# Optimization experiments

Measured on AMD Instinct MI355X. Metric: run time of the kernel, lower is better.

## Reference

```python
import jax, jax.numpy as jnp
import numpy as np

NUM_FACES = 400000  # total SMPL face count; faces[] and pix_to_face values lie in [-1, NUM_FACES)


def setup_inputs() -> dict:
    key = jax.random.key(0)
    k0, k1, k2, k3 = jax.random.split(key, 4)
    V, N, C, S = 4, 200000, 64, 512
    verts = jax.random.normal(k0, (N, 3), jnp.float32) * 0.5
    faces = jax.random.randint(k1, (N,), 0, NUM_FACES)
    # identity cameras looking at the point cloud from z=3 so projections land in-frame
    cam_rot = jnp.broadcast_to(jnp.eye(3, dtype=jnp.float32), (V, 3, 3))
    cam_trans = jnp.tile(jnp.array([0.0, 0.0, 3.0], jnp.float32), (V, 1))
    K = jnp.broadcast_to(
        jnp.array([[400.0, 0.0, 255.5], [0.0, 400.0, 255.5], [0.0, 0.0, 1.0]], jnp.float32),
        (V, 3, 3),
    )
    feature = jax.random.normal(k2, (V, C, S, S), jnp.float32)
    pix_to_face = jax.random.randint(k3, (V, S, S), -1, NUM_FACES).astype(jnp.int32)
    return dict(verts=verts, faces=faces, cam_rot=cam_rot, cam_trans=cam_trans, K=K,
                image_size=S, feature=feature, pix_to_face=pix_to_face)


def _project_xy(verts, K, R, t):
    # verts [N,3] -> pixel coords [N,2]
    cam = verts @ R.T + t  # [N,3]
    pix = cam @ K.T        # [N,3]
    return pix[:, :2] / pix[:, 2:]


def _bilinear_sample(feat, x, y, S):
    # feat [C,S,S]; torch grid_sample bilinear, align_corners=True, zero padding.
    # uv = loc/(S-1)*2-1 then grid_sample maps uv back to pixel coords, so the
    # sample location is exactly (x, y) in pixel space.
    x0 = jnp.floor(x); y0 = jnp.floor(y)
    x1 = x0 + 1.0;     y1 = y0 + 1.0
    wx1 = x - x0; wx0 = 1.0 - wx1
    wy1 = y - y0; wy0 = 1.0 - wy1

    def corner(xi, yi, w):
        valid = (xi >= 0) & (xi <= S - 1) & (yi >= 0) & (yi <= S - 1)
        xc = jnp.clip(xi, 0, S - 1).astype(jnp.int32)
        yc = jnp.clip(yi, 0, S - 1).astype(jnp.int32)
        return feat[:, yc, xc] * (w * valid)[None, :]  # [C,N]

    out = (corner(x0, y0, wx0 * wy0) + corner(x1, y0, wx1 * wy0)
           + corner(x0, y1, wx0 * wy1) + corner(x1, y1, wx1 * wy1))
    return out.T  # [N,C]


def _vis_mask(p2f, faces):
    # p2f [S,S] int (>=0 = foreground face id); faces [N] per-vertex face id.
    # Equivalent to torch.isin(faces, p2f[p2f>=0]) via a scatter membership table.
    flat = p2f.reshape(-1)
    idx = jnp.where(flat >= 0, flat, NUM_FACES)  # route background to sentinel slot
    table = jnp.zeros(NUM_FACES + 1, dtype=bool).at[idx].set(True)
    table = table.at[NUM_FACES].set(False)
    return table[faces]  # [N] bool


def reference(verts, faces, cam_rot, cam_trans, K, image_size, feature, pix_to_face):
    S = image_size

    def per_view(featv, Kv, Rv, tv, p2fv):
        xy = _project_xy(verts, Kv, Rv, tv)                    # [N,2]
        samp = _bilinear_sample(featv, xy[:, 0], xy[:, 1], S)  # [N,C]
        mask = _vis_mask(p2fv, faces)                          # [N]
        return samp, mask

    sampled, vmask = jax.vmap(per_view)(feature, K, cam_rot, cam_trans, pix_to_face)
    vm = vmask.astype(feature.dtype)                 # [V,N]
    # vertices invisible in all views: treat as visible everywhere (weight 1)
    vm = jnp.where(vm.sum(axis=0, keepdims=True) == 0, jnp.ones_like(vm), vm)
    out = (sampled * vm[:, :, None]).sum(axis=0) / vm.sum(axis=0)[:, None]  # [N,C]
    return out
```

## Files before the change

kernel.cpp:

```cpp
#include <hip/hip_runtime.h>

#define NUM_FACES 400000
#define NVIEW 4
#define NCHAN 64
#define IMGS 512
#define XT32 (IMGS / 32)
#define VPW 3

typedef float f32x4 __attribute__((ext_vector_type(4)));
typedef float f32x2 __attribute__((ext_vector_type(2)));

__device__ __forceinline__ unsigned short f2bf(float f) {
    unsigned int u = __float_as_uint(f);
    return (unsigned short)((u + 0x7FFFu + ((u >> 16) & 1u)) >> 16);
}

__device__ __forceinline__ void project_view(
    const float* __restrict__ cam_rot, const float* __restrict__ cam_trans,
    const float* __restrict__ Kmat, int v, float px, float py, float pz,
    float& x, float& y)
{
    const float* R  = cam_rot   + v * 9;
    const float* t  = cam_trans + v * 3;
    const float* Km = Kmat      + v * 9;
    float cx = R[0] * px + R[1] * py + R[2] * pz + t[0];
    float cy = R[3] * px + R[4] * py + R[5] * pz + t[1];
    float cz = R[6] * px + R[7] * py + R[8] * pz + t[2];
    float qx = Km[0] * cx + Km[1] * cy + Km[2] * cz;
    float qy = Km[3] * cx + Km[4] * cy + Km[5] * cz;
    float qz = Km[6] * cx + Km[7] * cy + Km[8] * cz;
    x = qx / qz;
    y = qy / qz;
}

__global__ void zero_ws_kernel(uint4* __restrict__ p, int n16) {
    int i = blockIdx.x * blockDim.x + threadIdx.x;
    if (i < n16) p[i] = make_uint4(0u, 0u, 0u, 0u);
}

__global__ void scatter_vis_kernel(const int4* __restrict__ p2f4,
                                   unsigned char* __restrict__ table) {
    const int pix4 = (NVIEW * IMGS * IMGS) / 4;
    int i = blockIdx.x * blockDim.x + threadIdx.x;
    if (i >= pix4) return;
    int4 f4 = p2f4[i];
    int v = i / ((IMGS * IMGS) / 4);
    unsigned char* tv = table + (size_t)v * NUM_FACES;
    if (f4.x >= 0) tv[f4.x] = 1;
    if (f4.y >= 0) tv[f4.y] = 1;
    if (f4.z >= 0) tv[f4.z] = 1;
    if (f4.w >= 0) tv[f4.w] = 1;
}

__global__ void vprep_kernel(const float* __restrict__ verts,
                             const int* __restrict__ faces,
                             const float* __restrict__ cam_rot,
                             const float* __restrict__ cam_trans,
                             const float* __restrict__ Kmat,
                             const unsigned char* __restrict__ table,
                             float* __restrict__ xyv,
                             unsigned char* __restrict__ vmask,
                             unsigned char* __restrict__ flags,
                             int n_verts) {
    int n = blockIdx.x * blockDim.x + threadIdx.x;
    if (n >= n_verts) return;
    float px = verts[n * 3 + 0], py = verts[n * 3 + 1], pz = verts[n * 3 + 2];
    int f = faces[n];
    unsigned int m = 0;
    float xy[8];
#pragma unroll
    for (int v = 0; v < NVIEW; ++v) {
        float x, y;
        project_view(cam_rot, cam_trans, Kmat, v, px, py, pz, x, y);
        xy[v * 2 + 0] = x;
        xy[v * 2 + 1] = y;
        if (f >= 0 && table[(size_t)v * NUM_FACES + f]) m |= (1u << v);
        int ix0 = (int)floorf(x), iy0 = (int)floorf(y);
        int bx  = min(max(ix0, 0), IMGS - 2);
        int ry0 = min(max(iy0, 0), IMGS - 1);
        int ry1 = min(max(iy0 + 1, 0), IMGS - 1);
        int ta = bx >> 5, tb = (bx + 1) >> 5;
        unsigned char* fv = flags + (size_t)v * IMGS * XT32;
        fv[ry0 * XT32 + ta] = 1;
        if (tb != ta) fv[ry0 * XT32 + tb] = 1;
        fv[ry1 * XT32 + ta] = 1;
        if (tb != ta) fv[ry1 * XT32 + tb] = 1;
    }
    if (m == 0) m = 15u;
    vmask[n] = (unsigned char)m;
    f32x4 a, b;
    a.x = xy[0]; a.y = xy[1]; a.z = xy[2]; a.w = xy[3];
    b.x = xy[4]; b.y = xy[5]; b.z = xy[6]; b.w = xy[7];
    f32x4* xp = reinterpret_cast<f32x4*>(xyv + (size_t)n * 8);
    xp[0] = a;
    xp[1] = b;
}

__global__ __launch_bounds__(256) void transpose_feat_kernel(
    const float* __restrict__ feature,
    unsigned short* __restrict__ feat_t,
    const unsigned char* __restrict__ flags)
{
    int b = blockIdx.x;
    int xt = b % XT32;
    int y  = (b / XT32) % IMGS;
    int v  = b / (XT32 * IMGS);
    if (!flags[((size_t)v * IMGS + y) * XT32 + xt]) return;

    __shared__ float tile[64 * 33];
    int x0 = xt * 32;
    const size_t SS = (size_t)IMGS * IMGS;
    int tid = threadIdx.x;

    const float* src = feature + (size_t)v * NCHAN * SS + (size_t)y * IMGS + x0;
#pragma unroll
    for (int i = 0; i < 2; ++i) {
        int lin = i * 256 + tid;
        int c  = lin >> 3;
        int xq = (lin & 7) * 4;
        f32x4 val = __builtin_nontemporal_load(
            reinterpret_cast<const f32x4*>(src + (size_t)c * SS + xq));
        tile[c * 33 + xq + 0] = val.x;
        tile[c * 33 + xq + 1] = val.y;
        tile[c * 33 + xq + 2] = val.z;
        tile[c * 33 + xq + 3] = val.w;
    }
    __syncthreads();

    unsigned short* dst = feat_t + (((size_t)v * IMGS + y) * IMGS + x0) * NCHAN;
#pragma unroll
    for (int i = 0; i < 2; ++i) {
        int lin = i * 256 + tid;
        int x  = lin >> 4;
        int c0 = (lin & 15) * 4;
        ushort4 w;
        w.x = f2bf(tile[(c0 + 0) * 33 + x]);
        w.y = f2bf(tile[(c0 + 1) * 33 + x]);
        w.z = f2bf(tile[(c0 + 2) * 33 + x]);
        w.w = f2bf(tile[(c0 + 3) * 33 + x]);
        *reinterpret_cast<ushort4*>(dst + (size_t)x * NCHAN + c0) = w;
    }
}

__global__ __launch_bounds__(256) void project_sample_bf16_kernel(
    const float* __restrict__ xyv,
    const unsigned char* __restrict__ vmask,
    const unsigned short* __restrict__ feat_t,
    float* __restrict__ out,
    int n_verts)
{
    int n0 = blockIdx.x * (4 * VPW) + (threadIdx.x >> 6) * VPW;
    int lane  = threadIdx.x & 63;
    int lhalf = lane >> 5;
    int cp    = lane & 31;

    unsigned int m[VPW];
    f32x4 xya[VPW], xyb[VPW];
#pragma unroll
    for (int s = 0; s < VPW; ++s) {
        int n = n0 + s;
        if (n < n_verts) {
            m[s] = vmask[n];
            const f32x4* xp = reinterpret_cast<const f32x4*>(xyv + (size_t)n * 8);
            xya[s] = xp[0];
            xyb[s] = xp[1];
        } else {
            m[s] = 0u;
            xya[s] = 0.f;
            xyb[s] = 0.f;
        }
    }

    unsigned int u0[VPW][NVIEW], u1[VPW][NVIEW];
    float w0[VPW][NVIEW], w1[VPW][NVIEW];
#pragma unroll
    for (int s = 0; s < VPW; ++s) {
        float xs[NVIEW] = {xya[s].x, xya[s].z, xyb[s].x, xyb[s].z};
        float ys[NVIEW] = {xya[s].y, xya[s].w, xyb[s].y, xyb[s].w};
#pragma unroll
        for (int v = 0; v < NVIEW; ++v) {
            u0[s][v] = 0u; u1[s][v] = 0u; w0[s][v] = 0.f; w1[s][v] = 0.f;
            if (m[s] & (1u << v)) {
                float x = xs[v], y = ys[v];
                float x0f = floorf(x), y0f = floorf(y);
                float wx1 = x - x0f, wx0 = 1.f - wx1;
                float wy1 = y - y0f, wy0 = 1.f - wy1;
                int ix0 = (int)x0f, iy0 = (int)y0f;
                int ix1 = ix0 + 1, iy1 = iy0 + 1;

                int bx = min(max(ix0, 0), IMGS - 2);
                int k  = bx + lhalf;
                float wxk = (k == ix0 ? wx0 : 0.f) + (k == ix1 ? wx1 : 0.f);

                int ry0 = min(max(iy0, 0), IMGS - 1);
                int ry1 = min(max(iy1, 0), IMGS - 1);
                float wyr0 = (iy0 >= 0 && iy0 <= IMGS - 1) ? wy0 : 0.f;
                float wyr1 = (iy1 >= 0 && iy1 <= IMGS - 1) ? wy1 : 0.f;

                const unsigned int* fv32 = reinterpret_cast<const unsigned int*>(
                    feat_t + (size_t)v * IMGS * IMGS * NCHAN);
                u0[s][v] = fv32[((size_t)ry0 * IMGS + bx) * 32 + lane];
                u1[s][v] = fv32[((size_t)ry1 * IMGS + bx) * 32 + lane];
                w0[s][v] = wxk * wyr0;
                w1[s][v] = wxk * wyr1;
            }
        }
    }

#pragma unroll
    for (int s = 0; s < VPW; ++s) {
        if (m[s] == 0u) continue;
        float accx = 0.f, accy = 0.f;
#pragma unroll
        for (int v = 0; v < NVIEW; ++v) {
            accx += __uint_as_float(u0[s][v] << 16) * w0[s][v]
                  + __uint_as_float(u1[s][v] << 16) * w1[s][v];
            accy += __uint_as_float(u0[s][v] & 0xFFFF0000u) * w0[s][v]
                  + __uint_as_float(u1[s][v] & 0xFFFF0000u) * w1[s][v];
        }
        accx += __shfl_xor(accx, 32, 64);
        accy += __shfl_xor(accy, 32, 64);
        if (lhalf == 0) {
            float r = 1.f / (float)__popc(m[s]);
            f32x2 o; o.x = accx * r; o.y = accy * r;
            __builtin_nontemporal_store(o,
                reinterpret_cast<f32x2*>(out + (size_t)(n0 + s) * NCHAN) + cp);
        }
    }
}

__global__ __launch_bounds__(256) void project_sample_direct_kernel(
    const float* __restrict__ verts,
    const int* __restrict__ faces,
    const float* __restrict__ cam_rot,
    const float* __restrict__ cam_trans,
    const float* __restrict__ Kmat,
    const float* __restrict__ feature,
    const unsigned char* __restrict__ table,
    float* __restrict__ out,
    int n_verts)
{
    int n = blockIdx.x * 4 + (threadIdx.x >> 6);
    int c = threadIdx.x & 63;
    if (n >= n_verts) return;

    float px = verts[n * 3 + 0], py = verts[n * 3 + 1], pz = verts[n * 3 + 2];
    int f = faces[n];
    float xs[NVIEW], ys[NVIEW], mask[NVIEW];
    float vsum = 0.f;
#pragma unroll
    for (int v = 0; v < NVIEW; ++v) {
        project_view(cam_rot, cam_trans, Kmat, v, px, py, pz, xs[v], ys[v]);
        float mm = (f >= 0 && table[(size_t)v * NUM_FACES + f]) ? 1.f : 0.f;
        mask[v] = mm; vsum += mm;
    }
    float wsum = vsum;
    if (vsum == 0.f) {
#pragma unroll
        for (int v = 0; v < NVIEW; ++v) mask[v] = 1.f;
        wsum = (float)NVIEW;
    }
    float acc = 0.f;
#pragma unroll
    for (int v = 0; v < NVIEW; ++v) {
        if (mask[v] == 0.f) continue;
        float x = xs[v], y = ys[v];
        float x0f = floorf(x), y0f = floorf(y);
        float wx1 = x - x0f, wx0 = 1.f - wx1;
        float wy1 = y - y0f, wy0 = 1.f - wy1;
        int x0 = (int)x0f, y0 = (int)y0f;
        int x1 = x0 + 1, y1 = y0 + 1;
        bool vx0 = (x0 >= 0) && (x0 <= IMGS - 1), vx1 = (x1 >= 0) && (x1 <= IMGS - 1);
        bool vy0 = (y0 >= 0) && (y0 <= IMGS - 1), vy1 = (y1 >= 0) && (y1 <= IMGS - 1);
        int cx0 = min(max(x0, 0), IMGS - 1), cx1 = min(max(x1, 0), IMGS - 1);
        int cy0 = min(max(y0, 0), IMGS - 1), cy1 = min(max(y1, 0), IMGS - 1);
        const float* fc = feature + ((size_t)v * NCHAN + c) * (size_t)(IMGS * IMGS);
        acc += fc[cy0 * IMGS + cx0] * (wx0 * wy0 * (float)(vx0 && vy0))
             + fc[cy0 * IMGS + cx1] * (wx1 * wy0 * (float)(vx1 && vy0))
             + fc[cy1 * IMGS + cx0] * (wx0 * wy1 * (float)(vx0 && vy1))
             + fc[cy1 * IMGS + cx1] * (wx1 * wy1 * (float)(vx1 && vy1));
    }
    out[(size_t)n * NCHAN + c] = acc / wsum;
}

extern "C" void kernel_launch(void* const* d_in, const int* in_sizes, int n_in,
                              void* d_out, int out_size, void* d_ws, size_t ws_size,
                              hipStream_t stream) {
    const float* verts     = (const float*)d_in[0];
    const int*   faces     = (const int*)d_in[1];
    const float* cam_rot   = (const float*)d_in[2];
    const float* cam_trans = (const float*)d_in[3];
    const float* Kmat      = (const float*)d_in[4];
    const float* feature   = (const float*)d_in[6];
    const int4*  p2f4      = (const int4*)d_in[7];
    float* out = (float*)d_out;

    int n_verts = in_sizes[1];

    size_t table_sz  = (size_t)NVIEW * NUM_FACES;
    size_t flag_off  = table_sz;
    size_t flag_sz   = (size_t)NVIEW * IMGS * XT32;
    size_t xyv_off   = (flag_off + flag_sz + 255) & ~(size_t)255;
    size_t xyv_sz    = (size_t)n_verts * 8 * sizeof(float);
    size_t vm_off    = xyv_off + xyv_sz;
    size_t vm_sz     = (size_t)n_verts;
    size_t feat_off  = (vm_off + vm_sz + 255) & ~(size_t)255;
    size_t feat_sz   = (size_t)NVIEW * IMGS * IMGS * NCHAN * sizeof(unsigned short);

    unsigned char* table  = (unsigned char*)d_ws;
    unsigned char* flags  = (unsigned char*)d_ws + flag_off;
    float*         xyv    = (float*)((char*)d_ws + xyv_off);
    unsigned char* vmask  = (unsigned char*)d_ws + vm_off;
    unsigned short* feat_t = (unsigned short*)((char*)d_ws + feat_off);

    const int pix4 = (NVIEW * IMGS * IMGS) / 4;

    if (ws_size >= feat_off + feat_sz) {
        int n16 = (int)((flag_off + flag_sz) / 16);
        zero_ws_kernel<<<(n16 + 255) / 256, 256, 0, stream>>>((uint4*)d_ws, n16);
        scatter_vis_kernel<<<(pix4 + 255) / 256, 256, 0, stream>>>(p2f4, table);
        vprep_kernel<<<(n_verts + 255) / 256, 256, 0, stream>>>(
            verts, faces, cam_rot, cam_trans, Kmat, table, xyv, vmask, flags, n_verts);
        transpose_feat_kernel<<<NVIEW * IMGS * XT32, 256, 0, stream>>>(
            feature, feat_t, flags);
        int sblocks = (n_verts + 4 * VPW - 1) / (4 * VPW);
        project_sample_bf16_kernel<<<sblocks, 256, 0, stream>>>(
            xyv, vmask, feat_t, out, n_verts);
    } else {
        int n16 = (int)(table_sz / 16);
        zero_ws_kernel<<<(n16 + 255) / 256, 256, 0, stream>>>((uint4*)d_ws, n16);
        scatter_vis_kernel<<<(pix4 + 255) / 256, 256, 0, stream>>>(p2f4, table);
        int nblocks = (n_verts + 3) / 4;
        project_sample_direct_kernel<<<nblocks, 256, 0, stream>>>(
            verts, faces, cam_rot, cam_trans, Kmat, feature, table, out, n_verts);
    }
}
```

Baseline: 147.2 us.

## Process a whole image row per block in transpose with prefetch of next tile

The transpose kernel now launches one block per image row instead of one per 32-pixel tile. Each block reads the row's 16 flag bytes at once, loops over only the flagged tiles, and prefetches the next tile's global loads while it converts and writes the current one. This removes the many blocks that only check a flag and exit, and overlaps load latency with the stores, at the cost of less parallelism per row and an extra barrier per tile. The sampling kernel also drops from 3 to 2 vertices per wave, which launches more blocks.

After: 143.7 us. 1.02x faster.

```diff
diff --git a/kernel.cpp b/kernel.cpp
--- a/kernel.cpp
+++ b/kernel.cpp
@@ -5,7 +5,7 @@
 #define NCHAN 64
 #define IMGS 512
 #define XT32 (IMGS / 32)
-#define VPW 3
+#define VPW 2
 
 typedef float f32x4 __attribute__((ext_vector_type(4)));
 typedef float f32x2 __attribute__((ext_vector_type(2)));
@@ -102,43 +102,70 @@
     const unsigned char* __restrict__ flags)
 {
     int b = blockIdx.x;
-    int xt = b % XT32;
-    int y  = (b / XT32) % IMGS;
-    int v  = b / (XT32 * IMGS);
-    if (!flags[((size_t)v * IMGS + y) * XT32 + xt]) return;
+    int y = b % IMGS;
+    int v = b / IMGS;
+
+    uint4 fw = *reinterpret_cast<const uint4*>(
+        flags + ((size_t)v * IMGS + y) * XT32);
+    unsigned int fm = 0;
+#pragma unroll
+    for (int t = 0; t < 16; ++t) {
+        unsigned int word = (t < 4) ? fw.x : (t < 8) ? fw.y : (t < 12) ? fw.z : fw.w;
+        if ((word >> ((t & 3) * 8)) & 0xFFu) fm |= (1u << t);
+    }
+    if (fm == 0) return;
 
     __shared__ float tile[64 * 33];
-    int x0 = xt * 32;
     const size_t SS = (size_t)IMGS * IMGS;
     int tid = threadIdx.x;
-
-    const float* src = feature + (size_t)v * NCHAN * SS + (size_t)y * IMGS + x0;
-#pragma unroll
-    for (int i = 0; i < 2; ++i) {
-        int lin = i * 256 + tid;
-        int c  = lin >> 3;
-        int xq = (lin & 7) * 4;
-        f32x4 val = __builtin_nontemporal_load(
-            reinterpret_cast<const f32x4*>(src + (size_t)c * SS + xq));
-        tile[c * 33 + xq + 0] = val.x;
-        tile[c * 33 + xq + 1] = val.y;
-        tile[c * 33 + xq + 2] = val.z;
-        tile[c * 33 + xq + 3] = val.w;
-    }
-    __syncthreads();
-
-    unsigned short* dst = feat_t + (((size_t)v * IMGS + y) * IMGS + x0) * NCHAN;
-#pragma unroll
-    for (int i = 0; i < 2; ++i) {
-        int lin = i * 256 + tid;
-        int x  = lin >> 4;
-        int c0 = (lin & 15) * 4;
-        ushort4 w;
-        w.x = f2bf(tile[(c0 + 0) * 33 + x]);
-        w.y = f2bf(tile[(c0 + 1) * 33 + x]);
-        w.z = f2bf(tile[(c0 + 2) * 33 + x]);
-        w.w = f2bf(tile[(c0 + 3) * 33 + x]);
-        *reinterpret_cast<ushort4*>(dst + (size_t)x * NCHAN + c0) = w;
+    const float* srcrow = feature + (size_t)v * NCHAN * SS + (size_t)y * IMGS;
+    unsigned short* dstrow = feat_t + ((size_t)v * IMGS + y) * IMGS * NCHAN;
+
+    int lc0 = tid >> 3;
+    int lxq = (tid & 7) * 4;
+
+    int cur = __ffs(fm) - 1;
+    f32x4 a = __builtin_nontemporal_load(
+        reinterpret_cast<const f32x4*>(srcrow + (size_t)lc0 * SS + cur * 32 + lxq));
+    f32x4 c = __builtin_nontemporal_load(
+        reinterpret_cast<const f32x4*>(srcrow + (size_t)(lc0 + 32) * SS + cur * 32 + lxq));
+
+    while (true) {
+        unsigned int above = (cur < 31) ? (fm & ~((2u << cur) - 1u)) : 0u;
+        int nxt = above ? (__ffs(above) - 1) : -1;
+
+        {
+            float* t0 = &tile[lc0 * 33 + lxq];
+            t0[0] = a.x; t0[1] = a.y; t0[2] = a.z; t0[3] = a.w;
+            float* t1 = &tile[(lc0 + 32) * 33 + lxq];
+            t1[0] = c.x; t1[1] = c.y; t1[2] = c.z; t1[3] = c.w;
+        }
+        __syncthreads();
+
+        f32x4 na, nc;
+        if (nxt >= 0) {
+            na = __builtin_nontemporal_load(
+                reinterpret_cast<const f32x4*>(srcrow + (size_t)lc0 * SS + nxt * 32 + lxq));
+            nc = __builtin_nontemporal_load(
+                reinterpret_cast<const f32x4*>(srcrow + (size_t)(lc0 + 32) * SS + nxt * 32 + lxq));
+        }
+
+        unsigned short* dst = dstrow + (size_t)(cur * 32) * NCHAN;
+#pragma unroll
+        for (int i = 0; i < 2; ++i) {
+            int lin = i * 256 + tid;
+            int x  = lin >> 4;
+            int c0 = (lin & 15) * 4;
+            ushort4 w;
+            w.x = f2bf(tile[(c0 + 0) * 33 + x]);
+            w.y = f2bf(tile[(c0 + 1) * 33 + x]);
+            w.z = f2bf(tile[(c0 + 2) * 33 + x]);
+            w.w = f2bf(tile[(c0 + 3) * 33 + x]);
+            *reinterpret_cast<ushort4*>(dst + (size_t)x * NCHAN + c0) = w;
+        }
+        if (nxt < 0) break;
+        __syncthreads();
+        a = na; c = nc; cur = nxt;
     }
 }
 
@@ -321,7 +348,7 @@
         scatter_vis_kernel<<<(pix4 + 255) / 256, 256, 0, stream>>>(p2f4, table);
         vprep_kernel<<<(n_verts + 255) / 256, 256, 0, stream>>>(
             verts, faces, cam_rot, cam_trans, Kmat, table, xyv, vmask, flags, n_verts);
-        transpose_feat_kernel<<<NVIEW * IMGS * XT32, 256, 0, stream>>>(
+        transpose_feat_kernel<<<NVIEW * IMGS, 256, 0, stream>>>(
             feature, feat_t, flags);
         int sblocks = (n_verts + 4 * VPW - 1) / (4 * VPW);
         project_sample_bf16_kernel<<<sblocks, 256, 0, stream>>>(
```
